# Kernel optimization log

Measured on AMD Instinct MI355X. Metric: run time of the kernel, lower is better.

The kernel has to match this reference:

```python
import jax, jax.numpy as jnp
import numpy as np

B, T, E, HH, V = 64, 128, 256, 256, 50000  # HH = hidden_size // 2 per LTC level
DT = 1.0


def setup_inputs() -> dict:
    key = jax.random.key(0)
    ks = jax.random.split(key, 12)
    s_in = 1.0 / np.sqrt(E)
    s_rec = 1.0 / np.sqrt(HH)
    tokens = jax.random.randint(ks[0], (B, T), 0, V, dtype=jnp.int32)
    emb = jax.random.normal(ks[1], (V, E), jnp.float32) * 0.02
    W_in0 = jax.random.normal(ks[2], (HH, E), jnp.float32) * s_in
    W_rec0 = jax.random.normal(ks[3], (HH, HH), jnp.float32) * s_rec
    b0 = jnp.zeros((HH,), jnp.float32)
    tau0 = jax.random.uniform(ks[4], (HH,), jnp.float32)
    # NCP sparsity mask: keep prob = 1 - sparsity_level = 0.5
    mask0 = (jax.random.uniform(ks[5], (HH, HH)) > 0.5).astype(jnp.float32)
    W_in1 = jax.random.normal(ks[6], (HH, HH), jnp.float32) * s_rec
    W_rec1 = jax.random.normal(ks[7], (HH, HH), jnp.float32) * s_rec
    b1 = jnp.zeros((HH,), jnp.float32)
    tau1 = jax.random.uniform(ks[8], (HH,), jnp.float32)
    mask1 = (jax.random.uniform(ks[9], (HH, HH)) > 0.5).astype(jnp.float32)
    return {"tokens": tokens, "emb": emb,
            "W_in0": W_in0, "W_rec0": W_rec0, "b0": b0, "tau0": tau0, "mask0": mask0,
            "W_in1": W_in1, "W_rec1": W_rec1, "b1": b1, "tau1": tau1, "mask1": mask1}


def _ltc_scan(x_seq, W_in, W_rec, mask, b, tau_raw):
    """LTC Euler integration over time. x_seq: [B, T, D] -> [B, T, H]."""
    tau = jax.nn.softplus(tau_raw) + 0.1        # positive time constants [H]
    Wr = W_rec * mask                            # NCP sparse recurrent weights
    x_proj = jnp.einsum('btd,hd->bth', x_seq, W_in) + b  # precompute input drive
    h0 = jnp.zeros((x_seq.shape[0], W_rec.shape[0]), x_seq.dtype)

    def step(h, xp_t):
        pre = xp_t + h @ Wr.T
        h_new = h + DT * ((-h + jnp.tanh(pre)) / tau)
        return h_new, h_new

    _, hs = jax.lax.scan(step, h0, jnp.swapaxes(x_proj, 0, 1))  # [T, B, H]
    return jnp.swapaxes(hs, 0, 1)


def reference(tokens, emb, W_in0, W_rec0, b0, tau0, mask0,
              W_in1, W_rec1, b1, tau1, mask1):
    x = emb[tokens]                                   # [B, T, E]
    h0_seq = _ltc_scan(x, W_in0, W_rec0, mask0, b0, tau0)      # level 0: [B, T, HH]
    h1_seq = _ltc_scan(h0_seq, W_in1, W_rec1, mask1, b1, tau1)  # level 1: [B, T, HH]
    return jnp.concatenate([h0_seq, h1_seq], axis=-1)  # [B, T, 2*HH] = hidden_size
```

## Files before the change

### kernel.cpp

```cpp
#include <hip/hip_runtime.h>
#include <hip/hip_bf16.h>

#define B_ 64
#define T_ 128
#define E_ 256
#define H_ 256
#define OW_ 512
#define LP 264
#define MAGIC 0x5AD00000u

typedef unsigned short ushort_t;
typedef __attribute__((ext_vector_type(8))) short bf16x8;
typedef __attribute__((ext_vector_type(4))) float f32x4;

#define LGKM_BARRIER() asm volatile("s_waitcnt lgkmcnt(0)\n\ts_barrier" ::: "memory")

#define PIN_FRAG(x) asm volatile("" : "+v"(x))

__device__ __forceinline__ ushort_t f2bf(float f) {
    unsigned int x = __float_as_uint(f);
    unsigned int r = x + 0x7FFFu + ((x >> 16) & 1u);
    return (ushort_t)(r >> 16);
}
__device__ __forceinline__ float fast_tanh(float x) {
    float e = __expf(2.0f * x);
    return 1.0f - 2.0f * __builtin_amdgcn_rcpf(e + 1.0f);
}
__device__ __forceinline__ bf16x8 load_bfrag(const float* W, const float* M,
                                             size_t base) {
    float4 a = *(const float4*)(W + base);
    float4 b = *(const float4*)(W + base + 4);
    if (M) {
        float4 ma = *(const float4*)(M + base);
        float4 mb = *(const float4*)(M + base + 4);
        a.x *= ma.x; a.y *= ma.y; a.z *= ma.z; a.w *= ma.w;
        b.x *= mb.x; b.y *= mb.y; b.z *= mb.z; b.w *= mb.w;
    }
    union { bf16x8 v; ushort_t u[8]; } r;
    r.u[0] = f2bf(a.x); r.u[1] = f2bf(a.y); r.u[2] = f2bf(a.z); r.u[3] = f2bf(a.w);
    r.u[4] = f2bf(b.x); r.u[5] = f2bf(b.y); r.u[6] = f2bf(b.z); r.u[7] = f2bf(b.w);
    return r.v;
}

__device__ __forceinline__ int a_off(int r, int k) {
    return ((k >> 5) << 9) + (((k >> 3) & 3) << 7) + (r << 3) + (k & 7);
}

template<bool FUSE, bool WAIT>
__device__ __forceinline__ void scan_core(
    int grp, ushort_t (*hb)[4096],
    const float* xp, int xp_stride, int xp_col,
    float* hout, int out_col,
    const float* Wrec, const float* Wmask, const float* tau_raw,
    const float* Wf, const float* bfv, float* xf,
    unsigned int* flag)
{
    const int tid  = threadIdx.x;
    const int lane = tid & 63;
    const int wv   = tid >> 6;
    const int quad = lane >> 4;
    const int l15  = lane & 15;
    const int n0   = wv * 32;
    const int bg   = grp * 8;

    bf16x8 Bf[2][8];
    #pragma unroll
    for (int tc = 0; tc < 2; ++tc)
        #pragma unroll
        for (int kk = 0; kk < 8; ++kk)
            Bf[tc][kk] = load_bfrag(Wrec, Wmask,
                (size_t)(n0 + tc * 16 + l15) * H_ + kk * 32 + quad * 8);

    bf16x8 Bf2[2][8];
    float  b2[2] = {0.f, 0.f};
    if (FUSE) {
        #pragma unroll
        for (int tc = 0; tc < 2; ++tc) {
            b2[tc] = bfv[n0 + tc * 16 + l15];
            #pragma unroll
            for (int kk = 0; kk < 8; ++kk)
                Bf2[tc][kk] = load_bfrag(Wf, nullptr,
                    (size_t)(n0 + tc * 16 + l15) * H_ + kk * 32 + quad * 8);
        }
    }

    float inv_tau[2], h_prev[2][2];
    float xp_c[2][2], xp_n[2][2], xp_nn[2][2];
    #pragma unroll
    for (int tc = 0; tc < 2; ++tc) {
        inv_tau[tc] = 1.0f / (logf(1.0f + __expf(tau_raw[n0 + tc * 16 + l15])) + 0.1f);
        #pragma unroll
        for (int reg = 0; reg < 2; ++reg) {
            h_prev[tc][reg] = 0.0f;
            xp_c[tc][reg] = xp_n[tc][reg] = xp_nn[tc][reg] = 0.0f;
        }
    }

    int woff[2][2];
    #pragma unroll
    for (int tc = 0; tc < 2; ++tc)
        #pragma unroll
        for (int reg = 0; reg < 2; ++reg)
            woff[tc][reg] = a_off(quad * 4 + reg, n0 + tc * 16 + l15);
    const int ab = ((l15 & 2) == 0) ? (lane * 8) : 0;

    if (!WAIT) {
        #pragma unroll
        for (int tc = 0; tc < 2; ++tc)
            #pragma unroll
            for (int reg = 0; reg < 2; ++reg) {
                const int b = bg + quad * 2 + reg;
                const int c = n0 + tc * 16 + l15;
                xp_c[tc][reg] = xp[(size_t)(b * T_ + 0) * xp_stride + xp_col + c];
                xp_n[tc][reg] = xp[(size_t)(b * T_ + 1) * xp_stride + xp_col + c];
            }
    }

    for (int i = tid; i < 4096; i += 512)
        ((unsigned int*)&hb[0][0])[i] = 0u;
    __syncthreads();

    const int tmax = FUSE ? T_ : (T_ - 1);
    for (int t = 0; t <= tmax; ++t) {
        const int rb = t & 1;

        #pragma unroll
        for (int tc = 0; tc < 2; ++tc)
            #pragma unroll
            for (int kk = 0; kk < 8; ++kk) {
                PIN_FRAG(Bf[tc][kk]);
                if (FUSE) PIN_FRAG(Bf2[tc][kk]);
            }

        if (WAIT && t < T_ && (t & 7) == 0) {
            if (tid == 0) {
                const unsigned need = (unsigned)(t >> 3) + 1u;
                for (;;) {
                    unsigned d = __hip_atomic_load(flag, __ATOMIC_ACQUIRE,
                                                   __HIP_MEMORY_SCOPE_AGENT) - MAGIC;
                    if (d >= need && d <= 16u) break;
                    __builtin_amdgcn_s_sleep(2);
                }
            }
            __syncthreads();
            #pragma unroll
            for (int tc = 0; tc < 2; ++tc)
                #pragma unroll
                for (int reg = 0; reg < 2; ++reg) {
                    const int b = bg + quad * 2 + reg;
                    xp_c[tc][reg] = xp[(size_t)(b * T_ + t) * xp_stride + xp_col
                                       + n0 + tc * 16 + l15];
                }
        }

        bf16x8 Af[8];
        {
            const ushort_t* a0 = &hb[rb][0];
            #pragma unroll
            for (int kk = 0; kk < 8; ++kk)
                Af[kk] = *(const bf16x8*)(a0 + ab + kk * 512);
        }

        if (t < T_) {
            if (WAIT) {
                if ((t & 7) != 7 && t + 1 < T_) {
                    #pragma unroll
                    for (int tc = 0; tc < 2; ++tc)
                        #pragma unroll
                        for (int reg = 0; reg < 2; ++reg) {
                            const int b = bg + quad * 2 + reg;
                            xp_n[tc][reg] = xp[(size_t)(b * T_ + t + 1) * xp_stride
                                               + xp_col + n0 + tc * 16 + l15];
                        }
                }
            } else if (t + 2 < T_) {
                #pragma unroll
                for (int tc = 0; tc < 2; ++tc)
                    #pragma unroll
                    for (int reg = 0; reg < 2; ++reg) {
                        const int b = bg + quad * 2 + reg;
                        xp_nn[tc][reg] = xp[(size_t)(b * T_ + t + 2) * xp_stride
                                            + xp_col + n0 + tc * 16 + l15];
                    }
            }

            f32x4 acc[2] = {{0.f,0.f,0.f,0.f},{0.f,0.f,0.f,0.f}};
            #pragma unroll
            for (int kk = 0; kk < 8; ++kk)
                #pragma unroll
                for (int tc = 0; tc < 2; ++tc)
                    acc[tc] = __builtin_amdgcn_mfma_f32_16x16x32_bf16(
                        Af[kk], Bf[tc][kk], acc[tc], 0, 0, 0);

            #pragma unroll
            for (int tc = 0; tc < 2; ++tc) {
                const int c = n0 + tc * 16 + l15;
                #pragma unroll
                for (int reg = 0; reg < 2; ++reg) {
                    const int b = bg + quad * 2 + reg;
                    const float pre = xp_c[tc][reg] + acc[tc][reg];
                    const float hn  = h_prev[tc][reg]
                                    + (fast_tanh(pre) - h_prev[tc][reg]) * inv_tau[tc];
                    h_prev[tc][reg] = hn;
                    hb[rb ^ 1][woff[tc][reg]] = f2bf(hn);
                    hout[(size_t)(b * T_ + t) * OW_ + out_col + c] = hn;
                }
            }
            if (WAIT) {
                if ((t & 7) != 7) {
                    #pragma unroll
                    for (int tc = 0; tc < 2; ++tc)
                        #pragma unroll
                        for (int reg = 0; reg < 2; ++reg)
                            xp_c[tc][reg] = xp_n[tc][reg];
                }
            } else {
                #pragma unroll
                for (int tc = 0; tc < 2; ++tc)
                    #pragma unroll
                    for (int reg = 0; reg < 2; ++reg) {
                        xp_c[tc][reg] = xp_n[tc][reg];
                        xp_n[tc][reg] = xp_nn[tc][reg];
                    }
            }
        }

        if (FUSE && t > 0) {
            f32x4 acc2[2];
            #pragma unroll
            for (int tc = 0; tc < 2; ++tc)
                acc2[tc] = (f32x4){b2[tc], b2[tc], b2[tc], b2[tc]};
            #pragma unroll
            for (int kk = 0; kk < 8; ++kk)
                #pragma unroll
                for (int tc = 0; tc < 2; ++tc)
                    acc2[tc] = __builtin_amdgcn_mfma_f32_16x16x32_bf16(
                        Af[kk], Bf2[tc][kk], acc2[tc], 0, 0, 0);
            #pragma unroll
            for (int tc = 0; tc < 2; ++tc) {
                const int c = n0 + tc * 16 + l15;
                #pragma unroll
                for (int reg = 0; reg < 2; ++reg) {
                    const int b = bg + quad * 2 + reg;
                    __hip_atomic_store(&xf[(size_t)(b * T_ + t - 1) * H_ + c],
                                       acc2[tc][reg],
                                       __ATOMIC_RELAXED, __HIP_MEMORY_SCOPE_AGENT);
                }
            }
        }

        if (FUSE && t > 0 && (t & 7) == 0) {
            __syncthreads();
            if (tid == 0)
                __hip_atomic_store(flag, MAGIC + (unsigned)(t >> 3),
                                   __ATOMIC_RELEASE, __HIP_MEMORY_SCOPE_AGENT);
        } else if (t < tmax) {
            LGKM_BARRIER();
        }
    }
}

__global__ __launch_bounds__(512, 1)
void ltc_dual(float* out,
              const float* __restrict__ Wr0, const float* __restrict__ m0,
              const float* __restrict__ t0,
              const float* __restrict__ Wi1, const float* __restrict__ b1v,
              const float* __restrict__ Wr1, const float* __restrict__ m1,
              const float* __restrict__ t1,
              float* xf, unsigned int* flags)
{
    __shared__ __align__(16) ushort_t hb[2][4096];
    if (blockIdx.x < 8)
        scan_core<true, false>(blockIdx.x, hb,
                               out, OW_, H_,
                               out, 0,
                               Wr0, m0, t0, Wi1, b1v, xf, flags + blockIdx.x);
    else
        scan_core<false, true>(blockIdx.x - 8, hb,
                               xf, H_, 0,
                               out, H_,
                               Wr1, m1, t1, nullptr, nullptr, nullptr,
                               flags + blockIdx.x - 8);
}

__global__ __launch_bounds__(512, 1)
void ltc_single(const float* xp, int xp_stride, int xp_col,
                float* hout, int out_col,
                const float* __restrict__ Wr, const float* __restrict__ mk,
                const float* __restrict__ tu)
{
    __shared__ __align__(16) ushort_t hb[2][4096];
    scan_core<false, false>(blockIdx.x, hb, xp, xp_stride, xp_col,
                            hout, out_col, Wr, mk, tu,
                            nullptr, nullptr, nullptr, nullptr);
}

__global__ __launch_bounds__(512, 2)
void proj_mfma(const float* __restrict__ src, int src_stride, int src_col,
               const int* __restrict__ tok,
               const float* __restrict__ Wi,
               const float* __restrict__ bias,
               float* __restrict__ dst, int dst_stride, int dst_col)
{
    const int tid  = threadIdx.x;
    const int lane = tid & 63;
    const int wv   = tid >> 6;
    const int quad = lane >> 4;
    const int l15  = lane & 15;
    const int n0   = wv * 32;

    __shared__ __align__(16) ushort_t As[32][LP];

    bf16x8 Bf[2][8];
    float  bj[2];
    #pragma unroll
    for (int tc = 0; tc < 2; ++tc) {
        const int n = n0 + tc * 16 + l15;
        bj[tc] = bias[n];
        #pragma unroll
        for (int kk = 0; kk < 8; ++kk)
            Bf[tc][kk] = load_bfrag(Wi, nullptr, (size_t)n * H_ + kk * 32 + quad * 8);
    }

    const int r0 = blockIdx.x * 32;
    {
        const int row = tid >> 4;
        const int seg = tid & 15;
        const size_t sb = (tok ? (size_t)tok[r0 + row] : (size_t)(r0 + row))
                          * src_stride + src_col + seg * 16;
        union { uint4 q[2]; ushort_t u[16]; } p;
        #pragma unroll
        for (int h = 0; h < 2; ++h) {
            float4 f0 = *(const float4*)(src + sb + h * 8);
            float4 f1 = *(const float4*)(src + sb + h * 8 + 4);
            p.u[h*8+0] = f2bf(f0.x); p.u[h*8+1] = f2bf(f0.y);
            p.u[h*8+2] = f2bf(f0.z); p.u[h*8+3] = f2bf(f0.w);
            p.u[h*8+4] = f2bf(f1.x); p.u[h*8+5] = f2bf(f1.y);
            p.u[h*8+6] = f2bf(f1.z); p.u[h*8+7] = f2bf(f1.w);
        }
        *(uint4*)&As[row][seg * 16]     = p.q[0];
        *(uint4*)&As[row][seg * 16 + 8] = p.q[1];
    }
    __syncthreads();

    #pragma unroll
    for (int rt = 0; rt < 2; ++rt) {
        bf16x8 Af[8];
        #pragma unroll
        for (int kk = 0; kk < 8; ++kk)
            Af[kk] = *(const bf16x8*)&As[rt * 16 + l15][kk * 32 + quad * 8];

        f32x4 acc[2] = {{bj[0],bj[0],bj[0],bj[0]}, {bj[1],bj[1],bj[1],bj[1]}};
        #pragma unroll
        for (int kk = 0; kk < 8; ++kk)
            #pragma unroll
            for (int tc = 0; tc < 2; ++tc)
                acc[tc] = __builtin_amdgcn_mfma_f32_16x16x32_bf16(
                    Af[kk], Bf[tc][kk], acc[tc], 0, 0, 0);

        #pragma unroll
        for (int tc = 0; tc < 2; ++tc) {
            const int c = n0 + tc * 16 + l15;
            #pragma unroll
            for (int reg = 0; reg < 4; ++reg) {
                const int r = r0 + rt * 16 + quad * 4 + reg;
                dst[(size_t)r * dst_stride + dst_col + c] = acc[tc][reg];
            }
        }
    }
}

extern "C" void kernel_launch(void* const* d_in, const int* in_sizes, int n_in,
                              void* d_out, int out_size, void* d_ws, size_t ws_size,
                              hipStream_t stream)
{
    const int*   tokens = (const int*)d_in[0];
    const float* emb    = (const float*)d_in[1];
    const float* W_in0  = (const float*)d_in[2];
    const float* W_rec0 = (const float*)d_in[3];
    const float* b0     = (const float*)d_in[4];
    const float* tau0   = (const float*)d_in[5];
    const float* mask0  = (const float*)d_in[6];
    const float* W_in1  = (const float*)d_in[7];
    const float* W_rec1 = (const float*)d_in[8];
    const float* b1     = (const float*)d_in[9];
    const float* tau1   = (const float*)d_in[10];
    const float* mask1  = (const float*)d_in[11];
    float* out = (float*)d_out;
    (void)in_sizes; (void)n_in; (void)out_size;

    const size_t xf_elems = (size_t)B_ * T_ * H_;
    const bool pipelined = ws_size >= xf_elems * sizeof(float) + 64;

    proj_mfma<<<dim3(256), dim3(512), 0, stream>>>(
        emb, E_, 0, tokens, W_in0, b0, out, OW_, H_);

    if (pipelined) {
        float* xf = (float*)d_ws;
        unsigned int* flags = (unsigned int*)((float*)d_ws + xf_elems);
        ltc_dual<<<dim3(16), dim3(512), 0, stream>>>(
            out, W_rec0, mask0, tau0, W_in1, b1, W_rec1, mask1, tau1, xf, flags);
    } else {
        ltc_single<<<dim3(8), dim3(512), 0, stream>>>(
            out, OW_, H_, out, 0, W_rec0, mask0, tau0);
        proj_mfma<<<dim3(256), dim3(512), 0, stream>>>(
            out, OW_, 0, nullptr, W_in1, b1, out, OW_, H_);
        ltc_single<<<dim3(8), dim3(512), 0, stream>>>(
            out, OW_, H_, out, H_, W_rec1, mask1, tau1);
    }
}
```

Measured before the change: 260.9 us.

## Fuse input projections into scan kernel, removing separate projection launch

Measured after the change: 295.8 us. 1.13x slower.

```diff
diff --git a/kernel.cpp b/kernel.cpp
--- a/kernel.cpp
+++ b/kernel.cpp
@@ -14,7 +14,6 @@
 typedef __attribute__((ext_vector_type(4))) float f32x4;
 
 #define LGKM_BARRIER() asm volatile("s_waitcnt lgkmcnt(0)\n\ts_barrier" ::: "memory")
-
 #define PIN_FRAG(x) asm volatile("" : "+v"(x))
 
 __device__ __forceinline__ ushort_t f2bf(float f) {
@@ -46,14 +45,19 @@
     return ((k >> 5) << 9) + (((k >> 3) & 3) << 7) + (r << 3) + (k & 7);
 }
 
-template<bool FUSE, bool WAIT>
-__device__ __forceinline__ void scan_core(
-    int grp, ushort_t (*hb)[4096],
-    const float* xp, int xp_stride, int xp_col,
-    float* hout, int out_col,
-    const float* Wrec, const float* Wmask, const float* tau_raw,
-    const float* Wf, const float* bfv, float* xf,
-    unsigned int* flag)
+__device__ __forceinline__ void stage_row(ushort_t* tile, int slot, int lane,
+                                          float4 v) {
+    union { unsigned long long q; ushort_t u[4]; } p;
+    p.u[0] = f2bf(v.x); p.u[1] = f2bf(v.y); p.u[2] = f2bf(v.z); p.u[3] = f2bf(v.w);
+    *(unsigned long long*)(tile + a_off(slot, lane * 4)) = p.q;
+}
+
+__device__ __forceinline__ void producer_core(
+    int grp, ushort_t (*hb)[4096], ushort_t (*eb)[4096],
+    const int* __restrict__ tokens, const float* __restrict__ emb,
+    const float* Wr0, const float* m0, const float* Wi0,
+    const float* b0v, const float* tau0,
+    float* out, unsigned int* flag)
 {
     const int tid  = threadIdx.x;
     const int lane = tid & 63;
@@ -62,37 +66,20 @@
     const int l15  = lane & 15;
     const int n0   = wv * 32;
     const int bg   = grp * 8;
-
-    bf16x8 Bf[2][8];
-    #pragma unroll
-    for (int tc = 0; tc < 2; ++tc)
-        #pragma unroll
-        for (int kk = 0; kk < 8; ++kk)
-            Bf[tc][kk] = load_bfrag(Wrec, Wmask,
-                (size_t)(n0 + tc * 16 + l15) * H_ + kk * 32 + quad * 8);
-
-    bf16x8 Bf2[2][8];
-    float  b2[2] = {0.f, 0.f};
-    if (FUSE) {
-        #pragma unroll
-        for (int tc = 0; tc < 2; ++tc) {
-            b2[tc] = bfv[n0 + tc * 16 + l15];
-            #pragma unroll
-            for (int kk = 0; kk < 8; ++kk)
-                Bf2[tc][kk] = load_bfrag(Wf, nullptr,
-                    (size_t)(n0 + tc * 16 + l15) * H_ + kk * 32 + quad * 8);
-        }
-    }
-
-    float inv_tau[2], h_prev[2][2];
-    float xp_c[2][2], xp_n[2][2], xp_nn[2][2];
+    const int slot = (wv >> 1) * 4 + (wv & 1);
+
+    bf16x8 Br[2][8], Bi[2][8];
+    float  b0r[2], inv_tau[2], h_prev[2][2];
     #pragma unroll
     for (int tc = 0; tc < 2; ++tc) {
-        inv_tau[tc] = 1.0f / (logf(1.0f + __expf(tau_raw[n0 + tc * 16 + l15])) + 0.1f);
-        #pragma unroll
-        for (int reg = 0; reg < 2; ++reg) {
-            h_prev[tc][reg] = 0.0f;
-            xp_c[tc][reg] = xp_n[tc][reg] = xp_nn[tc][reg] = 0.0f;
+        const int c = n0 + tc * 16 + l15;
+        b0r[tc] = b0v[c];
+        inv_tau[tc] = 1.0f / (logf(1.0f + __expf(tau0[c])) + 0.1f);
+        h_prev[tc][0] = h_prev[tc][1] = 0.f;
+        #pragma unroll
+        for (int kk = 0; kk < 8; ++kk) {
+            Br[tc][kk] = load_bfrag(Wr0, m0, (size_t)c * H_ + kk * 32 + quad * 8);
+            Bi[tc][kk] = load_bfrag(Wi0, nullptr, (size_t)c * E_ + kk * 32 + quad * 8);
         }
     }
 
@@ -104,183 +91,237 @@
             woff[tc][reg] = a_off(quad * 4 + reg, n0 + tc * 16 + l15);
     const int ab = ((l15 & 2) == 0) ? (lane * 8) : 0;
 
-    if (!WAIT) {
+    for (int i = tid; i < 4096; i += 512)
+        ((unsigned int*)&hb[0][0])[i] = 0u;
+    {
+        const int tk = tokens[(bg + wv) * T_ + 0];
+        float4 v = *(const float4*)(emb + (size_t)tk * E_ + lane * 4);
+        stage_row(eb[0], slot, lane, v);
+    }
+    __syncthreads();
+
+    for (int t = 0; t < T_; ++t) {
+        const int rb = t & 1;
+
         #pragma unroll
         for (int tc = 0; tc < 2; ++tc)
+            #pragma unroll
+            for (int kk = 0; kk < 8; ++kk) { PIN_FRAG(Br[tc][kk]); PIN_FRAG(Bi[tc][kk]); }
+
+        bf16x8 Af[8], Ef[8];
+        {
+            const ushort_t* a0 = &hb[rb][0];
+            const ushort_t* e0 = &eb[rb][0];
+            #pragma unroll
+            for (int kk = 0; kk < 8; ++kk) {
+                Af[kk] = *(const bf16x8*)(a0 + ab + kk * 512);
+                Ef[kk] = *(const bf16x8*)(e0 + ab + kk * 512);
+            }
+        }
+
+        float4 ev;
+        const bool have_next = (t + 1 < T_);
+        if (have_next) {
+            const int tk = tokens[(bg + wv) * T_ + t + 1];
+            ev = *(const float4*)(emb + (size_t)tk * E_ + lane * 4);
+        }
+
+        f32x4 acc0[2] = {{0.f,0.f,0.f,0.f},{0.f,0.f,0.f,0.f}};
+        f32x4 accp[2];
+        #pragma unroll
+        for (int tc = 0; tc < 2; ++tc)
+            accp[tc] = (f32x4){b0r[tc], b0r[tc], b0r[tc], b0r[tc]};
+        #pragma unroll
+        for (int kk = 0; kk < 8; ++kk)
+            #pragma unroll
+            for (int tc = 0; tc < 2; ++tc) {
+                acc0[tc] = __builtin_amdgcn_mfma_f32_16x16x32_bf16(
+                    Af[kk], Br[tc][kk], acc0[tc], 0, 0, 0);
+                accp[tc] = __builtin_amdgcn_mfma_f32_16x16x32_bf16(
+                    Ef[kk], Bi[tc][kk], accp[tc], 0, 0, 0);
+            }
+
+        if (have_next) stage_row(eb[rb ^ 1], slot, lane, ev);
+
+        #pragma unroll
+        for (int tc = 0; tc < 2; ++tc) {
+            const int c = n0 + tc * 16 + l15;
             #pragma unroll
             for (int reg = 0; reg < 2; ++reg) {
                 const int b = bg + quad * 2 + reg;
-                const int c = n0 + tc * 16 + l15;
-                xp_c[tc][reg] = xp[(size_t)(b * T_ + 0) * xp_stride + xp_col + c];
-                xp_n[tc][reg] = xp[(size_t)(b * T_ + 1) * xp_stride + xp_col + c];
-            }
-    }
+                const float pre = accp[tc][reg] + acc0[tc][reg];
+                const float hn  = h_prev[tc][reg]
+                                + (fast_tanh(pre) - h_prev[tc][reg]) * inv_tau[tc];
+                h_prev[tc][reg] = hn;
+                hb[rb ^ 1][woff[tc][reg]] = f2bf(hn);
+                __hip_atomic_store(&out[(size_t)(b * T_ + t) * OW_ + c], hn,
+                                   __ATOMIC_RELAXED, __HIP_MEMORY_SCOPE_AGENT);
+            }
+        }
+
+        if ((t & 7) == 7) {
+            __syncthreads();
+            if (tid == 0)
+                __hip_atomic_store(flag, MAGIC + (unsigned)((t + 1) >> 3),
+                                   __ATOMIC_RELEASE, __HIP_MEMORY_SCOPE_AGENT);
+        } else {
+            LGKM_BARRIER();
+        }
+    }
+}
+
+__device__ __forceinline__ void consumer_core(
+    int grp, ushort_t (*hb)[4096], ushort_t (*eb)[4096],
+    const float* Wr1, const float* m1, const float* Wi1,
+    const float* b1v, const float* tau1,
+    float* out, unsigned int* flag)
+{
+    const int tid  = threadIdx.x;
+    const int lane = tid & 63;
+    const int wv   = tid >> 6;
+    const int quad = lane >> 4;
+    const int l15  = lane & 15;
+    const int n0   = wv * 32;
+    const int bg   = grp * 8;
+    const int slot = (wv >> 1) * 4 + (wv & 1);
+
+    bf16x8 Br[2][8], Bi[2][8];
+    float  b1r[2], inv_tau[2], h_prev[2][2];
+    #pragma unroll
+    for (int tc = 0; tc < 2; ++tc) {
+        const int c = n0 + tc * 16 + l15;
+        b1r[tc] = b1v[c];
+        inv_tau[tc] = 1.0f / (logf(1.0f + __expf(tau1[c])) + 0.1f);
+        h_prev[tc][0] = h_prev[tc][1] = 0.f;
+        #pragma unroll
+        for (int kk = 0; kk < 8; ++kk) {
+            Br[tc][kk] = load_bfrag(Wr1, m1, (size_t)c * H_ + kk * 32 + quad * 8);
+            Bi[tc][kk] = load_bfrag(Wi1, nullptr, (size_t)c * H_ + kk * 32 + quad * 8);
+        }
+    }
+
+    int woff[2][2];
+    #pragma unroll
+    for (int tc = 0; tc < 2; ++tc)
+        #pragma unroll
+        for (int reg = 0; reg < 2; ++reg)
+            woff[tc][reg] = a_off(quad * 4 + reg, n0 + tc * 16 + l15);
+    const int ab = ((l15 & 2) == 0) ? (lane * 8) : 0;
 
     for (int i = tid; i < 4096; i += 512)
         ((unsigned int*)&hb[0][0])[i] = 0u;
+
+    if (tid == 0) {
+        for (;;) {
+            unsigned d = __hip_atomic_load(flag, __ATOMIC_ACQUIRE,
+                                           __HIP_MEMORY_SCOPE_AGENT) - MAGIC;
+            if (d >= 1u && d <= 16u) break;
+            __builtin_amdgcn_s_sleep(2);
+        }
+    }
     __syncthreads();
-
-    const int tmax = FUSE ? T_ : (T_ - 1);
-    for (int t = 0; t <= tmax; ++t) {
+    {
+        float4 v = *(const float4*)(out + (size_t)((bg + wv) * T_ + 0) * OW_
+                                    + lane * 4);
+        stage_row(eb[0], slot, lane, v);
+    }
+    __syncthreads();
+
+    for (int t = 0; t < T_; ++t) {
         const int rb = t & 1;
 
         #pragma unroll
         for (int tc = 0; tc < 2; ++tc)
             #pragma unroll
-            for (int kk = 0; kk < 8; ++kk) {
-                PIN_FRAG(Bf[tc][kk]);
-                if (FUSE) PIN_FRAG(Bf2[tc][kk]);
-            }
-
-        if (WAIT && t < T_ && (t & 7) == 0) {
-            if (tid == 0) {
-                const unsigned need = (unsigned)(t >> 3) + 1u;
-                for (;;) {
-                    unsigned d = __hip_atomic_load(flag, __ATOMIC_ACQUIRE,
-                                                   __HIP_MEMORY_SCOPE_AGENT) - MAGIC;
-                    if (d >= need && d <= 16u) break;
-                    __builtin_amdgcn_s_sleep(2);
-                }
-            }
-            __syncthreads();
-            #pragma unroll
-            for (int tc = 0; tc < 2; ++tc)
-                #pragma unroll
-                for (int reg = 0; reg < 2; ++reg) {
-                    const int b = bg + quad * 2 + reg;
-                    xp_c[tc][reg] = xp[(size_t)(b * T_ + t) * xp_stride + xp_col
-                                       + n0 + tc * 16 + l15];
-                }
-        }
-
-        bf16x8 Af[8];
+            for (int kk = 0; kk < 8; ++kk) { PIN_FRAG(Br[tc][kk]); PIN_FRAG(Bi[tc][kk]); }
+
+        bf16x8 Af[8], Ef[8];
         {
             const ushort_t* a0 = &hb[rb][0];
-            #pragma unroll
-            for (int kk = 0; kk < 8; ++kk)
+            const ushort_t* e0 = &eb[rb][0];
+            #pragma unroll
+            for (int kk = 0; kk < 8; ++kk) {
                 Af[kk] = *(const bf16x8*)(a0 + ab + kk * 512);
-        }
-
-        if (t < T_) {
-            if (WAIT) {
-                if ((t & 7) != 7 && t + 1 < T_) {
-                    #pragma unroll
-                    for (int tc = 0; tc < 2; ++tc)
-                        #pragma unroll
-                        for (int reg = 0; reg < 2; ++reg) {
-                            const int b = bg + quad * 2 + reg;
-                            xp_n[tc][reg] = xp[(size_t)(b * T_ + t + 1) * xp_stride
-                                               + xp_col + n0 + tc * 16 + l15];
-                        }
+                Ef[kk] = *(const bf16x8*)(e0 + ab + kk * 512);
+            }
+        }
+
+        const bool have_next = (t + 1 < T_);
+        const bool edge = ((t & 7) == 7);
+        float4 hv;
+        if (have_next && !edge)
+            hv = *(const float4*)(out + (size_t)((bg + wv) * T_ + t + 1) * OW_
+                                  + lane * 4);
+
+        f32x4 acc1[2] = {{0.f,0.f,0.f,0.f},{0.f,0.f,0.f,0.f}};
+        f32x4 acc2[2];
+        #pragma unroll
+        for (int tc = 0; tc < 2; ++tc)
+            acc2[tc] = (f32x4){b1r[tc], b1r[tc], b1r[tc], b1r[tc]};
+        #pragma unroll
+        for (int kk = 0; kk < 8; ++kk)
+            #pragma unroll
+            for (int tc = 0; tc < 2; ++tc) {
+                acc1[tc] = __builtin_amdgcn_mfma_f32_16x16x32_bf16(
+                    Af[kk], Br[tc][kk], acc1[tc], 0, 0, 0);
+                acc2[tc] = __builtin_amdgcn_mfma_f32_16x16x32_bf16(
+                    Ef[kk], Bi[tc][kk], acc2[tc], 0, 0, 0);
+            }
+
+        #pragma unroll
+        for (int tc = 0; tc < 2; ++tc) {
+            const int c = n0 + tc * 16 + l15;
+            #pragma unroll
+            for (int reg = 0; reg < 2; ++reg) {
+                const int b = bg + quad * 2 + reg;
+                const float pre = acc2[tc][reg] + acc1[tc][reg];
+                const float hn  = h_prev[tc][reg]
+                                + (fast_tanh(pre) - h_prev[tc][reg]) * inv_tau[tc];
+                h_prev[tc][reg] = hn;
+                hb[rb ^ 1][woff[tc][reg]] = f2bf(hn);
+                out[(size_t)(b * T_ + t) * OW_ + H_ + c] = hn;
+            }
+        }
+
+        if (have_next) {
+            if (edge) {
+                if (tid == 0) {
+                    const unsigned need = (unsigned)((t + 1) >> 3) + 1u;
+                    for (;;) {
+                        unsigned d = __hip_atomic_load(flag, __ATOMIC_ACQUIRE,
+                                                       __HIP_MEMORY_SCOPE_AGENT) - MAGIC;
+                        if (d >= need && d <= 16u) break;
+                        __builtin_amdgcn_s_sleep(2);
+                    }
                 }
-            } else if (t + 2 < T_) {
-                #pragma unroll
-                for (int tc = 0; tc < 2; ++tc)
-                    #pragma unroll
-                    for (int reg = 0; reg < 2; ++reg) {
-                        const int b = bg + quad * 2 + reg;
-                        xp_nn[tc][reg] = xp[(size_t)(b * T_ + t + 2) * xp_stride
-                                            + xp_col + n0 + tc * 16 + l15];
-                    }
-            }
-
-            f32x4 acc[2] = {{0.f,0.f,0.f,0.f},{0.f,0.f,0.f,0.f}};
-            #pragma unroll
-            for (int kk = 0; kk < 8; ++kk)
-                #pragma unroll
-                for (int tc = 0; tc < 2; ++tc)
-                    acc[tc] = __builtin_amdgcn_mfma_f32_16x16x32_bf16(
-                        Af[kk], Bf[tc][kk], acc[tc], 0, 0, 0);
-
-            #pragma unroll
-            for (int tc = 0; tc < 2; ++tc) {
-                const int c = n0 + tc * 16 + l15;
-                #pragma unroll
-                for (int reg = 0; reg < 2; ++reg) {
-                    const int b = bg + quad * 2 + reg;
-                    const float pre = xp_c[tc][reg] + acc[tc][reg];
-                    const float hn  = h_prev[tc][reg]
-                                    + (fast_tanh(pre) - h_prev[tc][reg]) * inv_tau[tc];
-                    h_prev[tc][reg] = hn;
-                    hb[rb ^ 1][woff[tc][reg]] = f2bf(hn);
-                    hout[(size_t)(b * T_ + t) * OW_ + out_col + c] = hn;
-                }
-            }
-            if (WAIT) {
-                if ((t & 7) != 7) {
-                    #pragma unroll
-                    for (int tc = 0; tc < 2; ++tc)
-                        #pragma unroll
-                        for (int reg = 0; reg < 2; ++reg)
-                            xp_c[tc][reg] = xp_n[tc][reg];
-                }
-            } else {
-                #pragma unroll
-                for (int tc = 0; tc < 2; ++tc)
-                    #pragma unroll
-                    for (int reg = 0; reg < 2; ++reg) {
-                        xp_c[tc][reg] = xp_n[tc][reg];
-                        xp_n[tc][reg] = xp_nn[tc][reg];
-                    }
-            }
-        }
-
-        if (FUSE && t > 0) {
-            f32x4 acc2[2];
-            #pragma unroll
-            for (int tc = 0; tc < 2; ++tc)
-                acc2[tc] = (f32x4){b2[tc], b2[tc], b2[tc], b2[tc]};
-            #pragma unroll
-            for (int kk = 0; kk < 8; ++kk)
-                #pragma unroll
-                for (int tc = 0; tc < 2; ++tc)
-                    acc2[tc] = __builtin_amdgcn_mfma_f32_16x16x32_bf16(
-                        Af[kk], Bf2[tc][kk], acc2[tc], 0, 0, 0);
-            #pragma unroll
-            for (int tc = 0; tc < 2; ++tc) {
-                const int c = n0 + tc * 16 + l15;
-                #pragma unroll
-                for (int reg = 0; reg < 2; ++reg) {
-                    const int b = bg + quad * 2 + reg;
-                    __hip_atomic_store(&xf[(size_t)(b * T_ + t - 1) * H_ + c],
-                                       acc2[tc][reg],
-                                       __ATOMIC_RELAXED, __HIP_MEMORY_SCOPE_AGENT);
-                }
-            }
-        }
-
-        if (FUSE && t > 0 && (t & 7) == 0) {
-            __syncthreads();
-            if (tid == 0)
-                __hip_atomic_store(flag, MAGIC + (unsigned)(t >> 3),
-                                   __ATOMIC_RELEASE, __HIP_MEMORY_SCOPE_AGENT);
-        } else if (t < tmax) {
+                __syncthreads();
+                hv = *(const float4*)(out + (size_t)((bg + wv) * T_ + t + 1) * OW_
+                                      + lane * 4);
+            }
+            stage_row(eb[rb ^ 1], slot, lane, hv);
             LGKM_BARRIER();
         }
     }
 }
 
 __global__ __launch_bounds__(512, 1)
-void ltc_dual(float* out,
-              const float* __restrict__ Wr0, const float* __restrict__ m0,
-              const float* __restrict__ t0,
-              const float* __restrict__ Wi1, const float* __restrict__ b1v,
-              const float* __restrict__ Wr1, const float* __restrict__ m1,
-              const float* __restrict__ t1,
-              float* xf, unsigned int* flags)
+void ltc_fused(const int* __restrict__ tokens, const float* __restrict__ emb,
+               const float* __restrict__ Wi0, const float* __restrict__ b0v,
+               const float* __restrict__ Wr0, const float* __restrict__ m0,
+               const float* __restrict__ t0,
+               const float* __restrict__ Wi1, const float* __restrict__ b1v,
+               const float* __restrict__ Wr1, const float* __restrict__ m1,
+               const float* __restrict__ t1,
+               float* out, unsigned int* flags)
 {
     __shared__ __align__(16) ushort_t hb[2][4096];
+    __shared__ __align__(16) ushort_t eb[2][4096];
     if (blockIdx.x < 8)
-        scan_core<true, false>(blockIdx.x, hb,
-                               out, OW_, H_,
-                               out, 0,
-                               Wr0, m0, t0, Wi1, b1v, xf, flags + blockIdx.x);
+        producer_core(blockIdx.x, hb, eb, tokens, emb,
+                      Wr0, m0, Wi0, b0v, t0, out, flags + blockIdx.x);
     else
-        scan_core<false, true>(blockIdx.x - 8, hb,
-                               xf, H_, 0,
-                               out, H_,
-                               Wr1, m1, t1, nullptr, nullptr, nullptr,
-                               flags + blockIdx.x - 8);
+        consumer_core(blockIdx.x - 8, hb, eb,
+                      Wr1, m1, Wi1, b1v, t1, out, flags + blockIdx.x - 8);
 }
 
 __global__ __launch_bounds__(512, 1)
@@ -290,9 +331,96 @@
                 const float* __restrict__ tu)
 {
     __shared__ __align__(16) ushort_t hb[2][4096];
-    scan_core<false, false>(blockIdx.x, hb, xp, xp_stride, xp_col,
-                            hout, out_col, Wr, mk, tu,
-                            nullptr, nullptr, nullptr, nullptr);
+    const int tid  = threadIdx.x;
+    const int lane = tid & 63;
+    const int wv   = tid >> 6;
+    const int quad = lane >> 4;
+    const int l15  = lane & 15;
+    const int n0   = wv * 32;
+    const int bg   = blockIdx.x * 8;
+
+    bf16x8 Bf[2][8];
+    #pragma unroll
+    for (int tc = 0; tc < 2; ++tc)
+        #pragma unroll
+        for (int kk = 0; kk < 8; ++kk)
+            Bf[tc][kk] = load_bfrag(Wr, mk,
+                (size_t)(n0 + tc * 16 + l15) * H_ + kk * 32 + quad * 8);
+
+    float inv_tau[2], h_prev[2][2], xp_c[2][2], xp_n[2][2], xp_nn[2][2];
+    #pragma unroll
+    for (int tc = 0; tc < 2; ++tc) {
+        inv_tau[tc] = 1.0f / (logf(1.0f + __expf(tu[n0 + tc * 16 + l15])) + 0.1f);
+        #pragma unroll
+        for (int reg = 0; reg < 2; ++reg) {
+            h_prev[tc][reg] = 0.f; xp_c[tc][reg] = xp_n[tc][reg] = xp_nn[tc][reg] = 0.f;
+            const int b = bg + quad * 2 + reg;
+            const int c = n0 + tc * 16 + l15;
+            xp_c[tc][reg] = xp[(size_t)(b * T_ + 0) * xp_stride + xp_col + c];
+            xp_n[tc][reg] = xp[(size_t)(b * T_ + 1) * xp_stride + xp_col + c];
+        }
+    }
+    int woff[2][2];
+    #pragma unroll
+    for (int tc = 0; tc < 2; ++tc)
+        #pragma unroll
+        for (int reg = 0; reg < 2; ++reg)
+            woff[tc][reg] = a_off(quad * 4 + reg, n0 + tc * 16 + l15);
+    const int ab = ((l15 & 2) == 0) ? (lane * 8) : 0;
+
+    for (int i = tid; i < 4096; i += 512)
+        ((unsigned int*)&hb[0][0])[i] = 0u;
+    __syncthreads();
+
+    for (int t = 0; t < T_; ++t) {
+        const int rb = t & 1;
+        bf16x8 Af[8];
+        {
+            const ushort_t* a0 = &hb[rb][0];
+            #pragma unroll
+            for (int kk = 0; kk < 8; ++kk)
+                Af[kk] = *(const bf16x8*)(a0 + ab + kk * 512);
+        }
+        if (t + 2 < T_) {
+            #pragma unroll
+            for (int tc = 0; tc < 2; ++tc)
+                #pragma unroll
+                for (int reg = 0; reg < 2; ++reg) {
+                    const int b = bg + quad * 2 + reg;
+                    xp_nn[tc][reg] = xp[(size_t)(b * T_ + t + 2) * xp_stride
+                                        + xp_col + n0 + tc * 16 + l15];
+                }
+        }
+        f32x4 acc[2] = {{0.f,0.f,0.f,0.f},{0.f,0.f,0.f,0.f}};
+        #pragma unroll
+        for (int kk = 0; kk < 8; ++kk)
+            #pragma unroll
+            for (int tc = 0; tc < 2; ++tc)
+                acc[tc] = __builtin_amdgcn_mfma_f32_16x16x32_bf16(
+                    Af[kk], Bf[tc][kk], acc[tc], 0, 0, 0);
+        #pragma unroll
+        for (int tc = 0; tc < 2; ++tc) {
+            const int c = n0 + tc * 16 + l15;
+            #pragma unroll
+            for (int reg = 0; reg < 2; ++reg) {
+                const int b = bg + quad * 2 + reg;
+                const float pre = xp_c[tc][reg] + acc[tc][reg];
+                const float hn  = h_prev[tc][reg]
+                                + (fast_tanh(pre) - h_prev[tc][reg]) * inv_tau[tc];
+                h_prev[tc][reg] = hn;
+                hb[rb ^ 1][woff[tc][reg]] = f2bf(hn);
+                hout[(size_t)(b * T_ + t) * OW_ + out_col + c] = hn;
+            }
+        }
+        #pragma unroll
+        for (int tc = 0; tc < 2; ++tc)
+            #pragma unroll
+            for (int reg = 0; reg < 2; ++reg) {
+                xp_c[tc][reg] = xp_n[tc][reg];
+                xp_n[tc][reg] = xp_nn[tc][reg];
+            }
+        if (t + 1 < T_) LGKM_BARRIER();
+    }
 }
 
 __global__ __launch_bounds__(512, 2)
@@ -389,18 +517,14 @@
     float* out = (float*)d_out;
     (void)in_sizes; (void)n_in; (void)out_size;
 
-    const size_t xf_elems = (size_t)B_ * T_ * H_;
-    const bool pipelined = ws_size >= xf_elems * sizeof(float) + 64;
-
-    proj_mfma<<<dim3(256), dim3(512), 0, stream>>>(
-        emb, E_, 0, tokens, W_in0, b0, out, OW_, H_);
-
-    if (pipelined) {
-        float* xf = (float*)d_ws;
-        unsigned int* flags = (unsigned int*)((float*)d_ws + xf_elems);
-        ltc_dual<<<dim3(16), dim3(512), 0, stream>>>(
-            out, W_rec0, mask0, tau0, W_in1, b1, W_rec1, mask1, tau1, xf, flags);
+    if (ws_size >= 64) {
+        unsigned int* flags = (unsigned int*)d_ws;
+        ltc_fused<<<dim3(16), dim3(512), 0, stream>>>(
+            tokens, emb, W_in0, b0, W_rec0, mask0, tau0,
+            W_in1, b1, W_rec1, mask1, tau1, out, flags);
     } else {
+        proj_mfma<<<dim3(256), dim3(512), 0, stream>>>(
+            emb, E_, 0, tokens, W_in0, b0, out, OW_, H_);
         ltc_single<<<dim3(8), dim3(512), 0, stream>>>(
             out, OW_, H_, out, 0, W_rec0, mask0, tau0);
         proj_mfma<<<dim3(256), dim3(512), 0, stream>>>(
```

## Fuse input projection into scan kernel with per-chunk readiness flags

Applied to the files above, without the earlier changes.

New measurement: 262.2 us. No clear change (+0.5%).

```diff
diff --git a/kernel.cpp b/kernel.cpp
--- a/kernel.cpp
+++ b/kernel.cpp
@@ -14,7 +14,6 @@
 typedef __attribute__((ext_vector_type(4))) float f32x4;
 
 #define LGKM_BARRIER() asm volatile("s_waitcnt lgkmcnt(0)\n\ts_barrier" ::: "memory")
-
 #define PIN_FRAG(x) asm volatile("" : "+v"(x))
 
 __device__ __forceinline__ ushort_t f2bf(float f) {
@@ -53,7 +52,7 @@
     float* hout, int out_col,
     const float* Wrec, const float* Wmask, const float* tau_raw,
     const float* Wf, const float* bfv, float* xf,
-    unsigned int* flag)
+    unsigned int* flag, const unsigned int* projf)
 {
     const int tid  = threadIdx.x;
     const int lane = tid & 63;
@@ -105,6 +104,18 @@
     const int ab = ((l15 & 2) == 0) ? (lane * 8) : 0;
 
     if (!WAIT) {
+        if (FUSE && projf != nullptr) {
+            if (tid < 8) {
+                const unsigned p = (unsigned)(bg + tid);
+                for (;;) {
+                    unsigned v = __hip_atomic_load(&projf[p], __ATOMIC_ACQUIRE,
+                                                   __HIP_MEMORY_SCOPE_AGENT);
+                    if (v == MAGIC) break;
+                    __builtin_amdgcn_s_sleep(2);
+                }
+            }
+            __syncthreads();
+        }
         #pragma unroll
         for (int tc = 0; tc < 2; ++tc)
             #pragma unroll
@@ -174,6 +185,19 @@
                         }
                 }
             } else if (t + 2 < T_) {
+                if (FUSE && projf != nullptr && ((t + 2) & 31) == 0) {
+                    if (tid < 8) {
+                        const unsigned p = (unsigned)(((t + 2) >> 5) * 64 + bg + tid);
+                        for (;;) {
+                            unsigned v = __hip_atomic_load(&projf[p],
+                                                           __ATOMIC_ACQUIRE,
+                                                           __HIP_MEMORY_SCOPE_AGENT);
+                            if (v == MAGIC) break;
+                            __builtin_amdgcn_s_sleep(2);
+                        }
+                    }
+                    __syncthreads();
+                }
                 #pragma unroll
                 for (int tc = 0; tc < 2; ++tc)
                     #pragma unroll
@@ -260,6 +284,122 @@
     }
 }
 
+__device__ __forceinline__ void proj_body(
+    int r0, const float* __restrict__ src, int src_stride, int src_col,
+    const int* __restrict__ tok,
+    const float* __restrict__ Wi, const float* __restrict__ bias,
+    float* __restrict__ dst, int dst_stride, int dst_col,
+    unsigned int* done, int done_idx)
+{
+    const int tid  = threadIdx.x;
+    const int lane = tid & 63;
+    const int wv   = tid >> 6;
+    const int quad = lane >> 4;
+    const int l15  = lane & 15;
+    const int n0   = wv * 32;
+
+    __shared__ __align__(16) ushort_t As[32][LP];
+
+    bf16x8 Bf[2][8];
+    float  bj[2];
+    #pragma unroll
+    for (int tc = 0; tc < 2; ++tc) {
+        const int n = n0 + tc * 16 + l15;
+        bj[tc] = bias[n];
+        #pragma unroll
+        for (int kk = 0; kk < 8; ++kk)
+            Bf[tc][kk] = load_bfrag(Wi, nullptr, (size_t)n * H_ + kk * 32 + quad * 8);
+    }
+
+    {
+        const int row = tid >> 4;
+        const int seg = tid & 15;
+        const size_t sb = (tok ? (size_t)tok[r0 + row] : (size_t)(r0 + row))
+                          * src_stride + src_col + seg * 16;
+        union { uint4 q[2]; ushort_t u[16]; } p;
+        #pragma unroll
+        for (int h = 0; h < 2; ++h) {
+            float4 f0 = *(const float4*)(src + sb + h * 8);
+            float4 f1 = *(const float4*)(src + sb + h * 8 + 4);
+            p.u[h*8+0] = f2bf(f0.x); p.u[h*8+1] = f2bf(f0.y);
+            p.u[h*8+2] = f2bf(f0.z); p.u[h*8+3] = f2bf(f0.w);
+            p.u[h*8+4] = f2bf(f1.x); p.u[h*8+5] = f2bf(f1.y);
+            p.u[h*8+6] = f2bf(f1.z); p.u[h*8+7] = f2bf(f1.w);
+        }
+        *(uint4*)&As[row][seg * 16]     = p.q[0];
+        *(uint4*)&As[row][seg * 16 + 8] = p.q[1];
+    }
+    __syncthreads();
+
+    #pragma unroll
+    for (int rt = 0; rt < 2; ++rt) {
+        bf16x8 Af[8];
+        #pragma unroll
+        for (int kk = 0; kk < 8; ++kk)
+            Af[kk] = *(const bf16x8*)&As[rt * 16 + l15][kk * 32 + quad * 8];
+
+        f32x4 acc[2] = {{bj[0],bj[0],bj[0],bj[0]}, {bj[1],bj[1],bj[1],bj[1]}};
+        #pragma unroll
+        for (int kk = 0; kk < 8; ++kk)
+            #pragma unroll
+            for (int tc = 0; tc < 2; ++tc)
+                acc[tc] = __builtin_amdgcn_mfma_f32_16x16x32_bf16(
+                    Af[kk], Bf[tc][kk], acc[tc], 0, 0, 0);
+
+        #pragma unroll
+        for (int tc = 0; tc < 2; ++tc) {
+            const int c = n0 + tc * 16 + l15;
+            #pragma unroll
+            for (int reg = 0; reg < 4; ++reg) {
+                const int r = r0 + rt * 16 + quad * 4 + reg;
+                if (done)
+                    __hip_atomic_store(&dst[(size_t)r * dst_stride + dst_col + c],
+                                       acc[tc][reg],
+                                       __ATOMIC_RELAXED, __HIP_MEMORY_SCOPE_AGENT);
+                else
+                    dst[(size_t)r * dst_stride + dst_col + c] = acc[tc][reg];
+            }
+        }
+    }
+
+    if (done) {
+        __syncthreads();
+        if (tid == 0)
+            __hip_atomic_store(&done[done_idx], MAGIC,
+                               __ATOMIC_RELEASE, __HIP_MEMORY_SCOPE_AGENT);
+    }
+}
+
+__global__ __launch_bounds__(512, 1)
+void ltc_all(const int* __restrict__ tokens, const float* __restrict__ emb,
+             const float* __restrict__ Wi0, const float* __restrict__ b0v,
+             const float* __restrict__ Wr0, const float* __restrict__ m0,
+             const float* __restrict__ t0,
+             const float* __restrict__ Wi1, const float* __restrict__ b1v,
+             const float* __restrict__ Wr1, const float* __restrict__ m1,
+             const float* __restrict__ t1,
+             float* out, float* xf, unsigned int* flags, unsigned int* projf)
+{
+    __shared__ __align__(16) ushort_t hb[2][4096];
+    if (blockIdx.x < 8)
+        scan_core<true, false>(blockIdx.x, hb,
+                               out, OW_, H_,
+                               out, 0,
+                               Wr0, m0, t0, Wi1, b1v, xf,
+                               flags + blockIdx.x, projf);
+    else if (blockIdx.x < 16)
+        scan_core<false, true>(blockIdx.x - 8, hb,
+                               xf, H_, 0,
+                               out, H_,
+                               Wr1, m1, t1, nullptr, nullptr, nullptr,
+                               flags + blockIdx.x - 8, nullptr);
+    else {
+        const int p  = blockIdx.x - 16;
+        const int r0 = (p & 63) * T_ + (p >> 6) * 32;
+        proj_body(r0, emb, E_, 0, tokens, Wi0, b0v, out, OW_, H_, projf, p);
+    }
+}
+
 __global__ __launch_bounds__(512, 1)
 void ltc_dual(float* out,
               const float* __restrict__ Wr0, const float* __restrict__ m0,
@@ -272,15 +412,14 @@
     __shared__ __align__(16) ushort_t hb[2][4096];
     if (blockIdx.x < 8)
         scan_core<true, false>(blockIdx.x, hb,
-                               out, OW_, H_,
-                               out, 0,
-                               Wr0, m0, t0, Wi1, b1v, xf, flags + blockIdx.x);
+                               out, OW_, H_, out, 0,
+                               Wr0, m0, t0, Wi1, b1v, xf,
+                               flags + blockIdx.x, nullptr);
     else
         scan_core<false, true>(blockIdx.x - 8, hb,
-                               xf, H_, 0,
-                               out, H_,
+                               xf, H_, 0, out, H_,
                                Wr1, m1, t1, nullptr, nullptr, nullptr,
-                               flags + blockIdx.x - 8);
+                               flags + blockIdx.x - 8, nullptr);
 }
 
 __global__ __launch_bounds__(512, 1)
@@ -292,7 +431,7 @@
     __shared__ __align__(16) ushort_t hb[2][4096];
     scan_core<false, false>(blockIdx.x, hb, xp, xp_stride, xp_col,
                             hout, out_col, Wr, mk, tu,
-                            nullptr, nullptr, nullptr, nullptr);
+                            nullptr, nullptr, nullptr, nullptr, nullptr);
 }
 
 __global__ __launch_bounds__(512, 2)
@@ -302,72 +441,8 @@
                const float* __restrict__ bias,
                float* __restrict__ dst, int dst_stride, int dst_col)
 {
-    const int tid  = threadIdx.x;
-    const int lane = tid & 63;
-    const int wv   = tid >> 6;
-    const int quad = lane >> 4;
-    const int l15  = lane & 15;
-    const int n0   = wv * 32;
-
-    __shared__ __align__(16) ushort_t As[32][LP];
-
-    bf16x8 Bf[2][8];
-    float  bj[2];
-    #pragma unroll
-    for (int tc = 0; tc < 2; ++tc) {
-        const int n = n0 + tc * 16 + l15;
-        bj[tc] = bias[n];
-        #pragma unroll
-        for (int kk = 0; kk < 8; ++kk)
-            Bf[tc][kk] = load_bfrag(Wi, nullptr, (size_t)n * H_ + kk * 32 + quad * 8);
-    }
-
-    const int r0 = blockIdx.x * 32;
-    {
-        const int row = tid >> 4;
-        const int seg = tid & 15;
-        const size_t sb = (tok ? (size_t)tok[r0 + row] : (size_t)(r0 + row))
-                          * src_stride + src_col + seg * 16;
-        union { uint4 q[2]; ushort_t u[16]; } p;
-        #pragma unroll
-        for (int h = 0; h < 2; ++h) {
-            float4 f0 = *(const float4*)(src + sb + h * 8);
-            float4 f1 = *(const float4*)(src + sb + h * 8 + 4);
-            p.u[h*8+0] = f2bf(f0.x); p.u[h*8+1] = f2bf(f0.y);
-            p.u[h*8+2] = f2bf(f0.z); p.u[h*8+3] = f2bf(f0.w);
-            p.u[h*8+4] = f2bf(f1.x); p.u[h*8+5] = f2bf(f1.y);
-            p.u[h*8+6] = f2bf(f1.z); p.u[h*8+7] = f2bf(f1.w);
-        }
-        *(uint4*)&As[row][seg * 16]     = p.q[0];
-        *(uint4*)&As[row][seg * 16 + 8] = p.q[1];
-    }
-    __syncthreads();
-
-    #pragma unroll
-    for (int rt = 0; rt < 2; ++rt) {
-        bf16x8 Af[8];
-        #pragma unroll
-        for (int kk = 0; kk < 8; ++kk)
-            Af[kk] = *(const bf16x8*)&As[rt * 16 + l15][kk * 32 + quad * 8];
-
-        f32x4 acc[2] = {{bj[0],bj[0],bj[0],bj[0]}, {bj[1],bj[1],bj[1],bj[1]}};
-        #pragma unroll
-        for (int kk = 0; kk < 8; ++kk)
-            #pragma unroll
-            for (int tc = 0; tc < 2; ++tc)
-                acc[tc] = __builtin_amdgcn_mfma_f32_16x16x32_bf16(
-                    Af[kk], Bf[tc][kk], acc[tc], 0, 0, 0);
-
-        #pragma unroll
-        for (int tc = 0; tc < 2; ++tc) {
-            const int c = n0 + tc * 16 + l15;
-            #pragma unroll
-            for (int reg = 0; reg < 4; ++reg) {
-                const int r = r0 + rt * 16 + quad * 4 + reg;
-                dst[(size_t)r * dst_stride + dst_col + c] = acc[tc][reg];
-            }
-        }
-    }
+    proj_body(blockIdx.x * 32, src, src_stride, src_col, tok, Wi, bias,
+              dst, dst_stride, dst_col, nullptr, 0);
 }
 
 extern "C" void kernel_launch(void* const* d_in, const int* in_sizes, int n_in,
@@ -390,17 +465,25 @@
     (void)in_sizes; (void)n_in; (void)out_size;
 
     const size_t xf_elems = (size_t)B_ * T_ * H_;
-    const bool pipelined = ws_size >= xf_elems * sizeof(float) + 64;
-
-    proj_mfma<<<dim3(256), dim3(512), 0, stream>>>(
-        emb, E_, 0, tokens, W_in0, b0, out, OW_, H_);
-
-    if (pipelined) {
+    const size_t xf_bytes = xf_elems * sizeof(float);
+
+    if (ws_size >= xf_bytes + 64 + 1024) {
         float* xf = (float*)d_ws;
-        unsigned int* flags = (unsigned int*)((float*)d_ws + xf_elems);
+        unsigned int* flags = (unsigned int*)((char*)d_ws + xf_bytes);
+        unsigned int* projf = (unsigned int*)((char*)d_ws + xf_bytes + 64);
+        ltc_all<<<dim3(272), dim3(512), 0, stream>>>(
+            tokens, emb, W_in0, b0, W_rec0, mask0, tau0,
+            W_in1, b1, W_rec1, mask1, tau1, out, xf, flags, projf);
+    } else if (ws_size >= xf_bytes + 64) {
+        float* xf = (float*)d_ws;
+        unsigned int* flags = (unsigned int*)((char*)d_ws + xf_bytes);
+        proj_mfma<<<dim3(256), dim3(512), 0, stream>>>(
+            emb, E_, 0, tokens, W_in0, b0, out, OW_, H_);
         ltc_dual<<<dim3(16), dim3(512), 0, stream>>>(
             out, W_rec0, mask0, tau0, W_in1, b1, W_rec1, mask1, tau1, xf, flags);
     } else {
+        proj_mfma<<<dim3(256), dim3(512), 0, stream>>>(
+            emb, E_, 0, tokens, W_in0, b0, out, OW_, H_);
         ltc_single<<<dim3(8), dim3(512), 0, stream>>>(
             out, OW_, H_, out, 0, W_rec0, mask0, tau0);
         proj_mfma<<<dim3(256), dim3(512), 0, stream>>>(
```
